# Kernel optimization log

Hardware: AMD Instinct MI355X
Metric: run time of the kernel (lower is better)

Reference implementation:

```python
import jax, jax.numpy as jnp
import numpy as np

B, L, D, H, NOC, OUT, FF = 32, 1024, 512, 512, 2000, 100, 256
ALPHA = 0.6


def setup_inputs() -> dict:
    key = jax.random.key(0)
    ks = jax.random.split(key, 12)
    s = lambda *sh: 1.0 / np.sqrt(sh[-1])
    inp = {
        "x": jax.random.normal(ks[0], (B, L, D), dtype=jnp.float32),
        "concepts": jax.random.randint(ks[1], (B,), 0, NOC),
        "emb": jax.random.normal(ks[2], (NOC, H), dtype=jnp.float32),
        # LSTM (single layer, torch gate order i,f,g,o), input size 2*D
        "Wih": jax.random.normal(ks[3], (4 * H, 2 * D), dtype=jnp.float32) * s(2 * D),
        "Whh": jax.random.normal(ks[4], (4 * H, H), dtype=jnp.float32) * s(H),
        "bih": jnp.zeros((4 * H,), dtype=jnp.float32),
        "bhh": jnp.zeros((4 * H,), dtype=jnp.float32),
        # mlp: Linear(D, D)
        "Wm": jax.random.normal(ks[5], (D, D), dtype=jnp.float32) * s(D),
        "bm": jnp.zeros((D,), dtype=jnp.float32),
        # linear_fit: Linear(H,256) -> ReLU -> (Dropout eval) -> Linear(256,OUT)
        "W1": jax.random.normal(ks[6], (FF, H), dtype=jnp.float32) * s(H),
        "b1": jnp.zeros((FF,), dtype=jnp.float32),
        "W2": jax.random.normal(ks[7], (OUT, FF), dtype=jnp.float32) * s(FF),
        "b2": jnp.zeros((OUT,), dtype=jnp.float32),
    }
    return inp


def _lstm(x, Wih, Whh, bih, bhh):
    # x: [B, L, 2D] -> hidden states [B, L, H]
    nH = Whh.shape[1]
    b = bih + bhh

    def step(carry, xt):
        h, c = carry
        gates = xt @ Wih.T + h @ Whh.T + b
        i, f, g, o = jnp.split(gates, 4, axis=-1)
        i, f, o = jax.nn.sigmoid(i), jax.nn.sigmoid(f), jax.nn.sigmoid(o)
        g = jnp.tanh(g)
        c = f * c + i * g
        h = o * jnp.tanh(c)
        return (h, c), h

    nB = x.shape[0]
    init = (jnp.zeros((nB, nH), x.dtype), jnp.zeros((nB, nH), x.dtype))
    _, hs = jax.lax.scan(step, init, jnp.swapaxes(x, 0, 1))
    return jnp.swapaxes(hs, 0, 1)


def reference(x, concepts, emb, Wih, Whh, bih, bhh, Wm, bm, W1, b1, W2, b2):
    nL = x.shape[1]
    # concept vector repeated over time, concat with code vectors
    cvec = emb[concepts][:, None, :]                      # [B,1,H]
    rnn_in = jnp.concatenate([x, jnp.broadcast_to(cvec, (x.shape[0], nL, cvec.shape[-1]))], axis=2)
    out = _lstm(rnn_in, Wih, Whh, bih, bhh)               # [B,L,H]

    mlp_out = x @ Wm.T + bm                                # [B,L,D]  (D == H)
    scores = jnp.einsum("btd,bsd->bts", mlp_out, out)     # [B,L,L]
    t_idx = jnp.arange(nL)
    dt = t_idx[:, None] - t_idx[None, :]                   # t - s
    mask = dt >= 0                                         # causal (s <= t)
    decay = jnp.exp(-ALPHA * jnp.maximum(dt, 0).astype(scores.dtype))
    scores = jnp.where(mask, scores * decay, -jnp.inf)
    attn = jax.nn.softmax(scores, axis=-1)                 # softmax over s in [0, t]
    weighted = jnp.einsum("bts,bsd->btd", attn, out)       # [B,L,H]

    h1 = jax.nn.relu(weighted @ W1.T + b1)                 # dropout is identity in eval
    res = h1 @ W2.T + b2                                   # [B,L,OUT]
    return res
```

## Files before the change

### kernel.cpp

```cpp
#include <hip/hip_runtime.h>
#include <hip/hip_bf16.h>
#include <stdint.h>

typedef unsigned short u16;
typedef unsigned int u32;
typedef unsigned long long u64;
typedef float f32x4 __attribute__((ext_vector_type(4)));
typedef short bf16x8 __attribute__((ext_vector_type(8)));
typedef unsigned u32x4 __attribute__((ext_vector_type(4)));

#define NB 32
#define NL 1024
#define ND 512
#define NH 512
#define G4 2048
#define NOUT 100
#define NFF 256
#define HSTR 528

__device__ inline u16 f2b(float f) {
    union { float f; unsigned i; } c; c.f = f;
    unsigned i = c.i;
    return (u16)((i + 0x7FFFu + ((i >> 16) & 1u)) >> 16);
}
__device__ inline bf16x8 cvt8(const float* __restrict__ p) {
    float4 a = *(const float4*)p;
    float4 b = *(const float4*)(p + 4);
    bf16x8 r;
    u16* h = (u16*)&r;
    h[0] = f2b(a.x); h[1] = f2b(a.y); h[2] = f2b(a.z); h[3] = f2b(a.w);
    h[4] = f2b(b.x); h[5] = f2b(b.y); h[6] = f2b(b.z); h[7] = f2b(b.w);
    return r;
}
__device__ inline f32x4 MF(bf16x8 a, bf16x8 b, f32x4 c) {
    return __builtin_amdgcn_mfma_f32_16x16x32_bf16(a, b, c, 0, 0, 0);
}
__device__ inline float tanh_f(float x) {
    float xx = fminf(fmaxf(x, -15.f), 15.f);
    float e = __expf(2.f * xx);
    return (e - 1.f) / (e + 1.f);
}
__device__ inline float sigm_f(float x) { return 1.f / (1.f + __expf(-x)); }

__device__ inline u32x4 ld_sc16(const u32x4* p) {
    u32x4 r;
    asm volatile("global_load_dwordx4 %0, %1, off sc0 sc1\n\t"
                 "s_waitcnt vmcnt(0)"
                 : "=&v"(r) : "v"(p) : "memory");
    return r;
}
__device__ inline void ld1_issue(const u32x4* p, u32x4& r) {
    asm volatile("global_load_dwordx4 %0, %1, off sc0 sc1"
                 : "=&v"(r) : "v"(p) : "memory");
}
__device__ inline void ld2_issue(const u32x4* p1, const u32x4* p2, u32x4& r1, u32x4& r2) {
    asm volatile("global_load_dwordx4 %0, %2, off sc0 sc1\n\t"
                 "global_load_dwordx4 %1, %3, off sc0 sc1"
                 : "=&v"(r1), "=&v"(r2) : "v"(p1), "v"(p2) : "memory");
}
__device__ inline void wait_vm1(u32x4& r1) {
    asm volatile("s_waitcnt vmcnt(0)" : "+v"(r1) :: "memory");
}
__device__ inline void wait_vm2(u32x4& r1, u32x4& r2) {
    asm volatile("s_waitcnt vmcnt(0)" : "+v"(r1), "+v"(r2) :: "memory");
}
__device__ inline void st_sc16(u32x4* p, u32x4 v) {
    asm volatile("global_store_dwordx4 %0, %1, off sc0 sc1"
                 :: "v"(p), "v"(v) : "memory");
}

__global__ __launch_bounds__(256) void k_wcast(const float* __restrict__ s,
                                               u16* __restrict__ d, int n4) {
    int i = blockIdx.x * 256 + threadIdx.x;
    if (i >= n4) return;
    float4 v = *(const float4*)&s[(size_t)i * 4];
    u64 pk = (u64)f2b(v.x) | ((u64)f2b(v.y) << 16) |
             ((u64)f2b(v.z) << 32) | ((u64)f2b(v.w) << 48);
    *(u64*)&d[(size_t)i * 4] = pk;
}

__global__ __launch_bounds__(256) void k_cbias(const float* __restrict__ emb,
                                               const int* __restrict__ concepts,
                                               const float* __restrict__ Wih,
                                               const float* __restrict__ bih,
                                               const float* __restrict__ bhh,
                                               float* __restrict__ cbias) {
    __shared__ float e[ND];
    int b = blockIdx.x;
    int r = blockIdx.y * 256 + threadIdx.x;
    int c = concepts[b];
    for (int i = threadIdx.x; i < ND; i += 256) e[i] = emb[c * ND + i];
    __syncthreads();
    const float* wrow = Wih + (size_t)r * 1024 + 512;
    float acc = 0.f;
#pragma unroll 4
    for (int k4 = 0; k4 < 128; k4++) {
        float4 wv = *(const float4*)&wrow[k4 * 4];
        acc += e[k4 * 4 + 0] * wv.x + e[k4 * 4 + 1] * wv.y +
               e[k4 * 4 + 2] * wv.z + e[k4 * 4 + 3] * wv.w;
    }
    cbias[b * G4 + r] = acc + bih[r] + bhh[r];
}

__global__ __launch_bounds__(256, 1) void k_lstm(const float* __restrict__ x,
                                                 const float* __restrict__ Wih,
                                                 const float* __restrict__ Whh,
                                                 const float* __restrict__ cbias,
                                                 u16* __restrict__ out,
                                                 u32x4* __restrict__ hx) {
    __shared__ __align__(16) u16 hsb[4 * HSTR];
    __shared__ __align__(16) u16 xb[2][4 * HSTR];
    __shared__ float gbuf[4 * 68];
    __shared__ float cb_lds[4 * 64];
    int g = blockIdx.x & 7, k = blockIdx.x >> 3;
    int tid = threadIdx.x;
    int w = tid >> 6, l = tid & 63, quad = l >> 4, lane = l & 15;
    int jj = k * 16;
    int b0 = g * 4;
    int rr = w, f0 = l * 8;

    bf16x8 bwx[16], bwh[16];
    {
        int n = l & 15, q4 = l >> 4;
        const float* wsrc = Wih + (size_t)(w * 512 + jj + n) * 1024 + q4 * 8;
        const float* hsrc = Whh + (size_t)(w * 512 + jj + n) * 512 + q4 * 8;
#pragma unroll
        for (int kk = 0; kk < 16; kk++) {
            bwx[kk] = cvt8(wsrc + kk * 32);
            bwh[kk] = cvt8(hsrc + kk * 32);
        }
        cb_lds[tid] = cbias[(size_t)(b0 + (tid >> 6)) * G4 +
                            (((tid >> 4) & 3) * 512) + jj + (tid & 15)];
        *(bf16x8*)&xb[0][rr * HSTR + f0] = cvt8(&x[((size_t)(b0 + rr) * NL) * ND + f0]);
    }

    u32x4* hxg = hx + (size_t)g * 768;
    int u1 = tid;
    int rm1 = u1 % 12;
    int lo1 = (rm1 / 3) * HSTR + (u1 / 12) * 16 + (rm1 % 3) * 6;
    int s1u = rm1 % 3;
    const u32x4* a1base = hxg + u1;
    bool two = (tid < 128);
    int u2 = 256 + tid;
    int rm2 = u2 % 12;
    int lo2 = (rm2 / 3) * HSTR + (u2 / 12) * 16 + (rm2 % 3) * 6;
    int s2u = rm2 % 3;
    const u32x4* a2base = hxg + u2;
    u32x4* myst = hxg + k * 12 + w * 3;

    float4 pa, pb;
    {
        const float* px = &x[((size_t)(b0 + rr) * NL + 1) * ND + f0];
        pa = *(const float4*)px; pb = *(const float4*)(px + 4);
    }
    __syncthreads();

    float c_reg = 0.f;

    for (int t = 0; t < NL; t++) {
        if (t + 1 < NL) {
            bf16x8 xv; u16* hh = (u16*)&xv;
            hh[0] = f2b(pa.x); hh[1] = f2b(pa.y); hh[2] = f2b(pa.z); hh[3] = f2b(pa.w);
            hh[4] = f2b(pb.x); hh[5] = f2b(pb.y); hh[6] = f2b(pb.z); hh[7] = f2b(pb.w);
            *(bf16x8*)&xb[(t + 1) & 1][rr * HSTR + f0] = xv;
        }
        u32x4 A1 = {}, A2 = {};
        const u32x4* A1p = a1base;
        const u32x4* A2p = a2base;
        if (t > 0) {
            int poff = ((t - 1) & 1) * 384;
            A1p = a1base + poff;
            A2p = a2base + poff;
            if (two) ld2_issue(A1p, A2p, A1, A2);
            else     ld1_issue(A1p, A1);
        }
        f32x4 ac0 = {}, ac1 = {}, ac2 = {}, ac3 = {};
#pragma unroll
        for (int kk = 0; kk < 16; kk += 4) {
            const u16* xbp = &xb[t & 1][(lane & 3) * HSTR + quad * 8];
            ac0 = MF(*(bf16x8*)&xbp[(kk + 0) * 32], bwx[kk + 0], ac0);
            ac1 = MF(*(bf16x8*)&xbp[(kk + 1) * 32], bwx[kk + 1], ac1);
            ac2 = MF(*(bf16x8*)&xbp[(kk + 2) * 32], bwx[kk + 2], ac2);
            ac3 = MF(*(bf16x8*)&xbp[(kk + 3) * 32], bwx[kk + 3], ac3);
        }
        if (t > 0) {
            if (two) wait_vm2(A1, A2); else wait_vm1(A1);
            __builtin_amdgcn_sched_barrier(0);
            int guard = 0;
            while (A1.w != (u32)t) {
                if (++guard > (1 << 22)) break;
                __builtin_amdgcn_s_sleep(1);
                A1 = ld_sc16(A1p);
            }
            if (two) {
                guard = 0;
                while (A2.w != (u32)t) {
                    if (++guard > (1 << 22)) break;
                    __builtin_amdgcn_s_sleep(1);
                    A2 = ld_sc16(A2p);
                }
            }
            *(u32*)&hsb[lo1] = A1.x; *(u32*)&hsb[lo1 + 2] = A1.y;
            if (s1u < 2) *(u32*)&hsb[lo1 + 4] = A1.z;
            if (two) {
                *(u32*)&hsb[lo2] = A2.x; *(u32*)&hsb[lo2 + 2] = A2.y;
                if (s2u < 2) *(u32*)&hsb[lo2 + 4] = A2.z;
            }
            __syncthreads();
        }
        if (t + 2 < NL) {
            const float* px = &x[((size_t)(b0 + rr) * NL + (t + 2)) * ND + f0];
            pa = *(const float4*)px; pb = *(const float4*)(px + 4);
        }
        if (t > 0) {
#pragma unroll
            for (int kk = 0; kk < 16; kk += 4) {
                const u16* hbp = &hsb[(lane & 3) * HSTR + quad * 8];
                ac0 = MF(*(bf16x8*)&hbp[(kk + 0) * 32], bwh[kk + 0], ac0);
                ac1 = MF(*(bf16x8*)&hbp[(kk + 1) * 32], bwh[kk + 1], ac1);
                ac2 = MF(*(bf16x8*)&hbp[(kk + 2) * 32], bwh[kk + 2], ac2);
                ac3 = MF(*(bf16x8*)&hbp[(kk + 3) * 32], bwh[kk + 3], ac3);
            }
        }
        f32x4 acc = (ac0 + ac1) + (ac2 + ac3);
        if (quad == 0) {
#pragma unroll
            for (int r = 0; r < 4; r++)
                gbuf[r * 68 + w * 16 + lane] = acc[r];
        }
        __syncthreads();
        {
            int j = l & 15;
            float gi = gbuf[w * 68 + 0 * 16 + j] + cb_lds[w * 64 + 0 * 16 + j];
            float gf = gbuf[w * 68 + 1 * 16 + j] + cb_lds[w * 64 + 1 * 16 + j];
            float gg = gbuf[w * 68 + 2 * 16 + j] + cb_lds[w * 64 + 2 * 16 + j];
            float go = gbuf[w * 68 + 3 * 16 + j] + cb_lds[w * 64 + 3 * 16 + j];
            float iv = sigm_f(gi), fv = sigm_f(gf), ov = sigm_f(go);
            float gv = tanh_f(gg);
            c_reg = fv * c_reg + iv * gv;
            unsigned hb32 = (unsigned)f2b(ov * tanh_f(c_reg));
            unsigned t0 = __shfl(hb32, l * 6 + 0), t1 = __shfl(hb32, l * 6 + 1);
            unsigned t2 = __shfl(hb32, l * 6 + 2), t3 = __shfl(hb32, l * 6 + 3);
            unsigned t4 = __shfl(hb32, l * 6 + 4), t5 = __shfl(hb32, l * 6 + 5);
            if (l < 3) {
                u32x4 U;
                U.x = t0 | (t1 << 16);
                U.y = t2 | (t3 << 16);
                U.z = (l < 2) ? (t4 | (t5 << 16)) : 0u;
                U.w = (u32)(t + 1);
                st_sc16(myst + (t & 1) * 384 + l, U);
            }
            unsigned v1 = __shfl_down(hb32, 1);
            unsigned v2 = __shfl_down(hb32, 2);
            unsigned v3 = __shfl_down(hb32, 3);
            if (l < 16 && (l & 3) == 0) {
                u64 pk = (u64)hb32 | ((u64)v1 << 16) | ((u64)v2 << 32) | ((u64)v3 << 48);
                *(u64*)&out[((size_t)(b0 + w) * NL + t) * NH + jj + l] = pk;
            }
        }
    }
}

__global__ __launch_bounds__(512) void k_attn(const float* __restrict__ x,
                                              const u16* __restrict__ Wmb,
                                              const float* __restrict__ bm,
                                              const u16* __restrict__ kv,
                                              const u16* __restrict__ W1b,
                                              const float* __restrict__ b1,
                                              const u16* __restrict__ W2b,
                                              const float* __restrict__ b2,
                                              float* __restrict__ outp) {
    __shared__ __align__(16) u16 Qs[16 * 520];
    __shared__ __align__(16) u16 Vt[512 * 40];
    __shared__ float Sbuf[16 * 33];
    __shared__ __align__(16) u16 Pbuf[16 * 40];
    __shared__ float alpha_s[16];
    __shared__ float l_s[16];
    int b = blockIdx.x, qt = blockIdx.y;
    int tid = threadIdx.x, w = tid >> 6, l = tid & 63, quad = l >> 4, lane = l & 15;

    {
        const float* xq = x + ((size_t)b * NL + qt * 16 + lane) * ND;
        f32x4 aq0 = {}, aq1 = {}, aq2 = {}, aq3 = {};
#pragma unroll 4
        for (int kk = 0; kk < 16; kk++) {
            bf16x8 a = cvt8(&xq[kk * 32 + quad * 8]);
            int koff = kk * 32 + quad * 8;
            aq0 = MF(a, *(const bf16x8*)&Wmb[(size_t)((w * 4 + 0) * 16 + lane) * ND + koff], aq0);
            aq1 = MF(a, *(const bf16x8*)&Wmb[(size_t)((w * 4 + 1) * 16 + lane) * ND + koff], aq1);
            aq2 = MF(a, *(const bf16x8*)&Wmb[(size_t)((w * 4 + 2) * 16 + lane) * ND + koff], aq2);
            aq3 = MF(a, *(const bf16x8*)&Wmb[(size_t)((w * 4 + 3) * 16 + lane) * ND + koff], aq3);
        }
        f32x4 aqs[4] = {aq0, aq1, aq2, aq3};
#pragma unroll
        for (int nt2 = 0; nt2 < 4; nt2++) {
            int n = (w * 4 + nt2) * 16 + lane;
            float bmv = bm[n];
#pragma unroll
            for (int r = 0; r < 4; r++)
                Qs[(quad * 4 + r) * 520 + n] = f2b(aqs[nt2][r] + bmv);
        }
    }
    float m_run = -30000.f, l_run = 0.f;
    f32x4 acc[4] = {};
    __syncthreads();

    int st_max = ((qt << 4) + 15) >> 5;
    for (int st = 0; st <= st_max; st++) {
        if (w < 2) {
            int ni = w;
            f32x4 s = {};
            const u16* krow = kv + ((size_t)b * NL + st * 32 + ni * 16 + lane) * NH;
#pragma unroll 4
            for (int kk = 0; kk < 16; kk++)
                s = MF(*(bf16x8*)&Qs[lane * 520 + kk * 32 + quad * 8],
                       *(const bf16x8*)&krow[kk * 32 + quad * 8], s);
            int scol = st * 32 + ni * 16 + lane;
#pragma unroll
            for (int r = 0; r < 4; r++) {
                int trow = (qt << 4) + quad * 4 + r;
                int dt = trow - scol;
                float v = (dt < 0) ? -30000.f : s[r] * __expf(-0.6f * (float)dt);
                Sbuf[(quad * 4 + r) * 33 + ni * 16 + lane] = v;
            }
        } else if (w >= 4) {
            int t2 = tid & 255;
            int srow = t2 >> 3, dseg = t2 & 7;
            const u16* vsrc = kv + ((size_t)b * NL + st * 32 + srow) * NH + dseg * 64;
#pragma unroll
            for (int i = 0; i < 8; i++) {
                union { uint4 v; u16 h[8]; } u;
                u.v = *(const uint4*)&vsrc[i * 8];
                int d0 = dseg * 64 + i * 8;
#pragma unroll
                for (int j2 = 0; j2 < 8; j2++) Vt[(d0 + j2) * 40 + srow] = u.h[j2];
            }
        }
        __syncthreads();
        if (tid < 64) {
            int m = tid >> 2, c0 = (tid & 3) * 8;
            float vmax = -30000.f;
#pragma unroll
            for (int i = 0; i < 8; i++) vmax = fmaxf(vmax, Sbuf[m * 33 + c0 + i]);
            vmax = fmaxf(vmax, __shfl_xor(vmax, 1));
            vmax = fmaxf(vmax, __shfl_xor(vmax, 2));
            float mnew = fmaxf(m_run, vmax);
            float al = __expf(m_run - mnew);
            float lsum = 0.f;
#pragma unroll
            for (int i = 0; i < 8; i++) {
                float p = __expf(Sbuf[m * 33 + c0 + i] - mnew);
                lsum += p;
                Pbuf[m * 40 + c0 + i] = f2b(p);
            }
            lsum += __shfl_xor(lsum, 1);
            lsum += __shfl_xor(lsum, 2);
            l_run = l_run * al + lsum;
            m_run = mnew;
            if ((tid & 3) == 0) { alpha_s[m] = al; l_s[m] = l_run; }
        }
        __syncthreads();
        {
            float a0 = alpha_s[quad * 4 + 0];
            float a1 = alpha_s[quad * 4 + 1];
            float a2 = alpha_s[quad * 4 + 2];
            float a3 = alpha_s[quad * 4 + 3];
            bf16x8 afrag = *(bf16x8*)&Pbuf[lane * 40 + quad * 8];
#pragma unroll
            for (int di = 0; di < 4; di++) {
                int dtile = w * 4 + di;
                f32x4 c = acc[di];
                c[0] *= a0; c[1] *= a1; c[2] *= a2; c[3] *= a3;
                acc[di] = MF(afrag, *(bf16x8*)&Vt[(dtile * 16 + lane) * 40 + quad * 8], c);
            }
        }
        __syncthreads();
    }

    u16* Wt = Vt;
    {
        float li0 = 1.f / l_s[quad * 4 + 0];
        float li1 = 1.f / l_s[quad * 4 + 1];
        float li2 = 1.f / l_s[quad * 4 + 2];
        float li3 = 1.f / l_s[quad * 4 + 3];
#pragma unroll
        for (int di = 0; di < 4; di++) {
            int col = (w * 4 + di) * 16 + lane;
            Wt[(quad * 4 + 0) * 520 + col] = f2b(acc[di][0] * li0);
            Wt[(quad * 4 + 1) * 520 + col] = f2b(acc[di][1] * li1);
            Wt[(quad * 4 + 2) * 520 + col] = f2b(acc[di][2] * li2);
            Wt[(quad * 4 + 3) * 520 + col] = f2b(acc[di][3] * li3);
        }
    }
    __syncthreads();
    u16* H1 = Qs;
    {
#pragma unroll
        for (int nt2 = 0; nt2 < 2; nt2++) {
            int n = (w * 2 + nt2) * 16 + lane;
            const u16* w1p = W1b + (size_t)n * ND;
            f32x4 a1 = {};
#pragma unroll 4
            for (int kk = 0; kk < 16; kk++)
                a1 = MF(*(bf16x8*)&Wt[lane * 520 + kk * 32 + quad * 8],
                        *(const bf16x8*)&w1p[kk * 32 + quad * 8], a1);
            float b1v = b1[n];
#pragma unroll
            for (int r = 0; r < 4; r++)
                H1[(quad * 4 + r) * 264 + n] = f2b(fmaxf(a1[r] + b1v, 0.f));
        }
    }
    __syncthreads();
    if (w < 7) {
        int n = w * 16 + lane;
        int nc = n < NOUT ? n : NOUT - 1;
        const u16* w2p = W2b + (size_t)nc * NFF;
        f32x4 a2 = {};
#pragma unroll
        for (int kk = 0; kk < 8; kk++)
            a2 = MF(*(bf16x8*)&H1[lane * 264 + kk * 32 + quad * 8],
                    *(const bf16x8*)&w2p[kk * 32 + quad * 8], a2);
        if (n < NOUT) {
            float b2v = b2[n];
#pragma unroll
            for (int r = 0; r < 4; r++)
                outp[((size_t)b * NL + (qt << 4) + quad * 4 + r) * NOUT + n] = a2[r] + b2v;
        }
    }
}

extern "C" void kernel_launch(void* const* d_in, const int* in_sizes, int n_in,
                              void* d_out, int out_size, void* d_ws, size_t ws_size,
                              hipStream_t stream) {
    const float* x        = (const float*)d_in[0];
    const int*   concepts = (const int*)d_in[1];
    const float* emb      = (const float*)d_in[2];
    const float* Wih      = (const float*)d_in[3];
    const float* Whh      = (const float*)d_in[4];
    const float* bih      = (const float*)d_in[5];
    const float* bhh      = (const float*)d_in[6];
    const float* Wm       = (const float*)d_in[7];
    const float* bm       = (const float*)d_in[8];
    const float* W1       = (const float*)d_in[9];
    const float* b1       = (const float*)d_in[10];
    const float* W2       = (const float*)d_in[11];
    const float* b2       = (const float*)d_in[12];
    float* outp = (float*)d_out;

    char* ws = (char*)d_ws;
    size_t off = 0;
    u16* lstm_out = (u16*)(ws + off); off += (size_t)NB * NL * NH * 2;
    float* cbias  = (float*)(ws + off); off += (size_t)NB * G4 * 4;
    u32x4* hx     = (u32x4*)(ws + off); off += (size_t)8 * 768 * 16;
    u16* Wmb      = (u16*)(ws + off); off += (size_t)ND * ND * 2;
    u16* W1b      = (u16*)(ws + off); off += (size_t)NFF * ND * 2;
    u16* W2b      = (u16*)(ws + off); off += (size_t)NOUT * NFF * 2;

    (void)hipMemsetAsync(hx, 0, (size_t)8 * 768 * 16, stream);
    k_wcast<<<(ND * ND / 4 + 255) / 256, 256, 0, stream>>>(Wm, Wmb, ND * ND / 4);
    k_wcast<<<(NFF * ND / 4 + 255) / 256, 256, 0, stream>>>(W1, W1b, NFF * ND / 4);
    k_wcast<<<(NOUT * NFF / 4 + 255) / 256, 256, 0, stream>>>(W2, W2b, NOUT * NFF / 4);
    k_cbias<<<dim3(NB, G4 / 256), 256, 0, stream>>>(emb, concepts, Wih, bih, bhh, cbias);
    k_lstm<<<256, 256, 0, stream>>>(x, Wih, Whh, cbias, lstm_out, hx);
    k_attn<<<dim3(NB, NL / 16), 512, 0, stream>>>(x, Wmb, bm, lstm_out, W1b, b1, W2b, b2, outp);
}
```

Before: 2.419 ms.

## Interleave LSTM gate rows so gate math stays in registers, drop LDS barrier

Reorders the Wih/Whh weight rows held in each wave so that the four gates (i,f,g,o) for one hidden unit land in adjacent MFMA output columns. The gate values can then be gathered with xor-shuffles inside the wave instead of going through an LDS gate buffer and a second __syncthreads per timestep. The cross-block h exchange packet also changes to a uniform 4-values-per-slot layout (512 slots per parity). Every thread now issues two polled loads, which removes the divergent one-load/two-load branching, but each packet carries 4 bf16 values instead of 6, so more packets are exchanged. The bias is held in registers instead of LDS.

```diff
diff --git a/kernel.cpp b/kernel.cpp
--- a/kernel.cpp
+++ b/kernel.cpp
@@ -49,17 +49,10 @@
                  : "=&v"(r) : "v"(p) : "memory");
     return r;
 }
-__device__ inline void ld1_issue(const u32x4* p, u32x4& r) {
-    asm volatile("global_load_dwordx4 %0, %1, off sc0 sc1"
-                 : "=&v"(r) : "v"(p) : "memory");
-}
 __device__ inline void ld2_issue(const u32x4* p1, const u32x4* p2, u32x4& r1, u32x4& r2) {
     asm volatile("global_load_dwordx4 %0, %2, off sc0 sc1\n\t"
                  "global_load_dwordx4 %1, %3, off sc0 sc1"
                  : "=&v"(r1), "=&v"(r2) : "v"(p1), "v"(p2) : "memory");
-}
-__device__ inline void wait_vm1(u32x4& r1) {
-    asm volatile("s_waitcnt vmcnt(0)" : "+v"(r1) :: "memory");
 }
 __device__ inline void wait_vm2(u32x4& r1, u32x4& r2) {
     asm volatile("s_waitcnt vmcnt(0)" : "+v"(r1), "+v"(r2) :: "memory");
@@ -110,43 +103,43 @@
                                                  u32x4* __restrict__ hx) {
     __shared__ __align__(16) u16 hsb[4 * HSTR];
     __shared__ __align__(16) u16 xb[2][4 * HSTR];
-    __shared__ float gbuf[4 * 68];
-    __shared__ float cb_lds[4 * 64];
     int g = blockIdx.x & 7, k = blockIdx.x >> 3;
     int tid = threadIdx.x;
     int w = tid >> 6, l = tid & 63, quad = l >> 4, lane = l & 15;
     int jj = k * 16;
     int b0 = g * 4;
     int rr = w, f0 = l * 8;
+    int gidx = l & 3;
+    int cidx = lane >> 2;
 
     bf16x8 bwx[16], bwh[16];
+    float cbv0, cbv1, cbv2, cbv3;
     {
-        int n = l & 15, q4 = l >> 4;
-        const float* wsrc = Wih + (size_t)(w * 512 + jj + n) * 1024 + q4 * 8;
-        const float* hsrc = Whh + (size_t)(w * 512 + jj + n) * 512 + q4 * 8;
+        int n = lane;
+        int wrow = (n & 3) * 512 + jj + w * 4 + (n >> 2);
+        int q4 = l >> 4;
+        const float* wsrc = Wih + (size_t)wrow * 1024 + q4 * 8;
+        const float* hsrc = Whh + (size_t)wrow * 512 + q4 * 8;
 #pragma unroll
         for (int kk = 0; kk < 16; kk++) {
             bwx[kk] = cvt8(wsrc + kk * 32);
             bwh[kk] = cvt8(hsrc + kk * 32);
         }
-        cb_lds[tid] = cbias[(size_t)(b0 + (tid >> 6)) * G4 +
-                            (((tid >> 4) & 3) * 512) + jj + (tid & 15)];
+        size_t cb = (size_t)(b0 + gidx) * G4 + jj + w * 4 + cidx;
+        cbv0 = cbias[cb + 0 * 512];
+        cbv1 = cbias[cb + 1 * 512];
+        cbv2 = cbias[cb + 2 * 512];
+        cbv3 = cbias[cb + 3 * 512];
         *(bf16x8*)&xb[0][rr * HSTR + f0] = cvt8(&x[((size_t)(b0 + rr) * NL) * ND + f0]);
     }
 
-    u32x4* hxg = hx + (size_t)g * 768;
-    int u1 = tid;
-    int rm1 = u1 % 12;
-    int lo1 = (rm1 / 3) * HSTR + (u1 / 12) * 16 + (rm1 % 3) * 6;
-    int s1u = rm1 % 3;
-    const u32x4* a1base = hxg + u1;
-    bool two = (tid < 128);
-    int u2 = 256 + tid;
-    int rm2 = u2 % 12;
-    int lo2 = (rm2 / 3) * HSTR + (u2 / 12) * 16 + (rm2 % 3) * 6;
-    int s2u = rm2 % 3;
-    const u32x4* a2base = hxg + u2;
-    u32x4* myst = hxg + k * 12 + w * 3;
+    u32x4* hxg = hx + (size_t)g * 1024;
+    int p1 = tid >> 4, r1 = (tid >> 2) & 3, w1 = tid & 3;
+    int lo1 = r1 * HSTR + p1 * 16 + w1 * 4;
+    int lo2 = lo1 + 256;
+    const u32x4* a1base = hxg + tid;
+    const u32x4* a2base = hxg + 256 + tid;
+    u32x4* myst = hxg + k * 16 + w;
 
     float4 pa, pb;
     {
@@ -168,11 +161,10 @@
         const u32x4* A1p = a1base;
         const u32x4* A2p = a2base;
         if (t > 0) {
-            int poff = ((t - 1) & 1) * 384;
+            int poff = ((t - 1) & 1) * 512;
             A1p = a1base + poff;
             A2p = a2base + poff;
-            if (two) ld2_issue(A1p, A2p, A1, A2);
-            else     ld1_issue(A1p, A1);
+            ld2_issue(A1p, A2p, A1, A2);
         }
         f32x4 ac0 = {}, ac1 = {}, ac2 = {}, ac3 = {};
 #pragma unroll
@@ -184,7 +176,7 @@
             ac3 = MF(*(bf16x8*)&xbp[(kk + 3) * 32], bwx[kk + 3], ac3);
         }
         if (t > 0) {
-            if (two) wait_vm2(A1, A2); else wait_vm1(A1);
+            wait_vm2(A1, A2);
             __builtin_amdgcn_sched_barrier(0);
             int guard = 0;
             while (A1.w != (u32)t) {
@@ -192,26 +184,20 @@
                 __builtin_amdgcn_s_sleep(1);
                 A1 = ld_sc16(A1p);
             }
-            if (two) {
-                guard = 0;
-                while (A2.w != (u32)t) {
-                    if (++guard > (1 << 22)) break;
-                    __builtin_amdgcn_s_sleep(1);
-                    A2 = ld_sc16(A2p);
-                }
+            guard = 0;
+            while (A2.w != (u32)t) {
+                if (++guard > (1 << 22)) break;
+                __builtin_amdgcn_s_sleep(1);
+                A2 = ld_sc16(A2p);
             }
             *(u32*)&hsb[lo1] = A1.x; *(u32*)&hsb[lo1 + 2] = A1.y;
-            if (s1u < 2) *(u32*)&hsb[lo1 + 4] = A1.z;
-            if (two) {
-                *(u32*)&hsb[lo2] = A2.x; *(u32*)&hsb[lo2 + 2] = A2.y;
-                if (s2u < 2) *(u32*)&hsb[lo2 + 4] = A2.z;
-            }
-            __syncthreads();
+            *(u32*)&hsb[lo2] = A2.x; *(u32*)&hsb[lo2 + 2] = A2.y;
         }
         if (t + 2 < NL) {
             const float* px = &x[((size_t)(b0 + rr) * NL + (t + 2)) * ND + f0];
             pa = *(const float4*)px; pb = *(const float4*)(px + 4);
         }
+        __syncthreads();
         if (t > 0) {
 #pragma unroll
             for (int kk = 0; kk < 16; kk += 4) {
@@ -223,39 +209,42 @@
             }
         }
         f32x4 acc = (ac0 + ac1) + (ac2 + ac3);
-        if (quad == 0) {
-#pragma unroll
-            for (int r = 0; r < 4; r++)
-                gbuf[r * 68 + w * 16 + lane] = acc[r];
-        }
-        __syncthreads();
         {
-            int j = l & 15;
-            float gi = gbuf[w * 68 + 0 * 16 + j] + cb_lds[w * 64 + 0 * 16 + j];
-            float gf = gbuf[w * 68 + 1 * 16 + j] + cb_lds[w * 64 + 1 * 16 + j];
-            float gg = gbuf[w * 68 + 2 * 16 + j] + cb_lds[w * 64 + 2 * 16 + j];
-            float go = gbuf[w * 68 + 3 * 16 + j] + cb_lds[w * 64 + 3 * 16 + j];
+            float a0 = acc[0], a1 = acc[1], a2 = acc[2], a3 = acc[3];
+            auto ext = [&](int i) {
+                float t01 = (i & 1) ? a1 : a0;
+                float t23 = (i & 1) ? a3 : a2;
+                return (i & 2) ? t23 : t01;
+            };
+            float own = ext(gidx);
+            float r1v = __shfl_xor(ext(gidx ^ 1), 1);
+            float r2v = __shfl_xor(ext(gidx ^ 2), 2);
+            float r3v = __shfl_xor(ext(gidx ^ 3), 3);
+            auto pick = [&](int i) {
+                float t01 = (i & 1) ? r1v : own;
+                float t23 = (i & 1) ? r3v : r2v;
+                return (i & 2) ? t23 : t01;
+            };
+            float gi = pick(gidx) + cbv0;
+            float gf = pick(gidx ^ 1) + cbv1;
+            float gg = pick(gidx ^ 2) + cbv2;
+            float go = pick(gidx ^ 3) + cbv3;
             float iv = sigm_f(gi), fv = sigm_f(gf), ov = sigm_f(go);
             float gv = tanh_f(gg);
             c_reg = fv * c_reg + iv * gv;
-            unsigned hb32 = (unsigned)f2b(ov * tanh_f(c_reg));
-            unsigned t0 = __shfl(hb32, l * 6 + 0), t1 = __shfl(hb32, l * 6 + 1);
-            unsigned t2 = __shfl(hb32, l * 6 + 2), t3 = __shfl(hb32, l * 6 + 3);
-            unsigned t4 = __shfl(hb32, l * 6 + 4), t5 = __shfl(hb32, l * 6 + 5);
-            if (l < 3) {
+            unsigned h32 = (unsigned)f2b(ov * tanh_f(c_reg));
+            unsigned s1 = __shfl(h32, (l & 3) + 4);
+            unsigned s2 = __shfl(h32, (l & 3) + 8);
+            unsigned s3 = __shfl(h32, (l & 3) + 12);
+            if (l < 4) {
                 u32x4 U;
-                U.x = t0 | (t1 << 16);
-                U.y = t2 | (t3 << 16);
-                U.z = (l < 2) ? (t4 | (t5 << 16)) : 0u;
+                U.x = h32 | (s1 << 16);
+                U.y = s2 | (s3 << 16);
+                U.z = 0u;
                 U.w = (u32)(t + 1);
-                st_sc16(myst + (t & 1) * 384 + l, U);
-            }
-            unsigned v1 = __shfl_down(hb32, 1);
-            unsigned v2 = __shfl_down(hb32, 2);
-            unsigned v3 = __shfl_down(hb32, 3);
-            if (l < 16 && (l & 3) == 0) {
-                u64 pk = (u64)hb32 | ((u64)v1 << 16) | ((u64)v2 << 32) | ((u64)v3 << 48);
-                *(u64*)&out[((size_t)(b0 + w) * NL + t) * NH + jj + l] = pk;
+                st_sc16(myst + (t & 1) * 512 + l * 4, U);
+                *(u64*)&out[((size_t)(b0 + l) * NL + t) * NH + jj + w * 4] =
+                    (u64)U.x | ((u64)U.y << 32);
             }
         }
     }
@@ -451,12 +440,12 @@
     size_t off = 0;
     u16* lstm_out = (u16*)(ws + off); off += (size_t)NB * NL * NH * 2;
     float* cbias  = (float*)(ws + off); off += (size_t)NB * G4 * 4;
-    u32x4* hx     = (u32x4*)(ws + off); off += (size_t)8 * 768 * 16;
+    u32x4* hx     = (u32x4*)(ws + off); off += (size_t)8 * 1024 * 16;
     u16* Wmb      = (u16*)(ws + off); off += (size_t)ND * ND * 2;
     u16* W1b      = (u16*)(ws + off); off += (size_t)NFF * ND * 2;
     u16* W2b      = (u16*)(ws + off); off += (size_t)NOUT * NFF * 2;
 
-    (void)hipMemsetAsync(hx, 0, (size_t)8 * 768 * 16, stream);
+    (void)hipMemsetAsync(hx, 0, (size_t)8 * 1024 * 16, stream);
     k_wcast<<<(ND * ND / 4 + 255) / 256, 256, 0, stream>>>(Wm, Wmb, ND * ND / 4);
     k_wcast<<<(NFF * ND / 4 + 255) / 256, 256, 0, stream>>>(W1, W1b, NFF * ND / 4);
     k_wcast<<<(NOUT * NFF / 4 + 255) / 256, 256, 0, stream>>>(W2, W2b, NOUT * NFF / 4);
```

Result: faster. 2.206 ms (-8.8%).
